# Optimization experiments

Measured on AMD Instinct MI355X. Metric: run time of the kernel, lower is better.

Reference implementation:

```python
import jax, jax.numpy as jnp
import numpy as np

B, S, D = 4, 4096, 1024
EXPAND = 2
D_INNER = EXPAND * D          # 2048
D_CONV = 4
CHUNK = 64
H = 16
DH = D // H                   # 64
EPS = 1e-5


def setup_inputs() -> dict:
    key = jax.random.key(0)
    ks = jax.random.split(key, 10)
    s = 0.02
    return {
        "x": jax.random.normal(ks[0], (B, S, D), jnp.float32),
        "norm_w": jnp.ones((D,), jnp.float32),
        "w_up": jax.random.normal(ks[1], (D, D_INNER), jnp.float32) * s,
        "w_gate": jax.random.normal(ks[2], (D, D_INNER), jnp.float32) * s,
        "w_down": jax.random.normal(ks[3], (D_INNER, D), jnp.float32) * s,
        "conv_w": jax.random.normal(ks[4], (D_INNER, 1, D_CONV), jnp.float32) * s,
        "conv_b": jnp.zeros((D_INNER,), jnp.float32),
        "wq": jax.random.normal(ks[5], (D, D), jnp.float32) * s,
        "wk": jax.random.normal(ks[6], (D, D), jnp.float32) * s,
        "wv": jax.random.normal(ks[7], (D, D), jnp.float32) * s,
        "wo": jax.random.normal(ks[8], (D, D), jnp.float32) * s,
    }


def rmsnorm(x, w):
    var = jnp.mean(jnp.square(x.astype(jnp.float32)), axis=-1, keepdims=True)
    return (x * jax.lax.rsqrt(var + EPS).astype(x.dtype)) * w


def causal_dwconv(x, w, b):
    # x: [B, S, C] -> depthwise causal conv along S
    y = jax.lax.conv_general_dilated(
        x.transpose(0, 2, 1), w,
        window_strides=(1,), padding=[(D_CONV - 1, 0)],
        feature_group_count=D_INNER,
        dimension_numbers=("NCH", "OIH", "NCH"))
    return (y + b[None, :, None]).transpose(0, 2, 1)


def hebbian_memory(h, wq, wk, wv, wo):
    # chunked Hebbian associative memory: M += phi(k)^T v, read y = phi(q) M (+ intra-chunk causal)
    phi = lambda t: jax.nn.elu(t) + 1.0
    q = phi((h @ wq).reshape(B, S, H, DH)) * (DH ** -0.5)
    k = phi((h @ wk).reshape(B, S, H, DH))
    v = (h @ wv).reshape(B, S, H, DH)

    def to_chunks(t):  # [B,S,H,DH] -> [N, B, H, CHUNK, DH]
        return t.reshape(B, S // CHUNK, CHUNK, H, DH).transpose(1, 0, 3, 2, 4)

    qc, kc, vc = to_chunks(q), to_chunks(k), to_chunks(v)
    mask = jnp.tril(jnp.ones((CHUNK, CHUNK), bool))

    def step(M, inp):
        qb, kb, vb = inp                                   # [B,H,C,DH]
        inter = jnp.einsum("bhcd,bhde->bhce", qb, M)       # read from past memory
        sc = jnp.einsum("bhcd,bhed->bhce", qb, kb)
        sc = jnp.where(mask, sc, 0.0)                      # causal intra-chunk Hebbian read
        intra = jnp.einsum("bhce,bhed->bhcd", sc, vb)
        M = M + jnp.einsum("bhcd,bhce->bhde", kb, vb)      # Hebbian outer-product write
        return M, inter + intra

    M0 = jnp.zeros((B, H, DH, DH), h.dtype)
    _, y = jax.lax.scan(step, M0, (qc, kc, vc))            # y: [N,B,H,C,DH]
    y = y.transpose(1, 0, 3, 2, 4).reshape(B, S, D)
    return y @ wo


def reference(x, norm_w, w_up, w_gate, w_down, conv_w, conv_b, wq, wk, wv, wo):
    normed = rmsnorm(x, norm_w)
    val = jax.nn.silu(causal_dwconv(normed @ w_up, conv_w, conv_b))   # conv local mixing
    h = (jax.nn.silu(normed @ w_gate) * val) @ w_down                 # gated MLP
    out = hebbian_memory(h, wq, wk, wv, wo)                           # associative memory
    return x + out
```

## Files before the change

### kernel.cpp

```cpp
#include <hip/hip_runtime.h>
#include <hip/hip_fp16.h>
#include <cstdint>

#define NRALL 16384
#define DM    1024
#define DI    2048
#define SEQL  4096

typedef _Float16 f16;
typedef _Float16 f16x8 __attribute__((ext_vector_type(8)));
typedef _Float16 f16x4 __attribute__((ext_vector_type(4)));
typedef float    f32x4 __attribute__((ext_vector_type(4)));

__device__ __forceinline__ float phi_f(float t)  { return t > 0.0f ? t + 1.0f : __expf(t); }
__device__ __forceinline__ float silu_f(float t) { return t / (1.0f + __expf(-t)); }

#define GLDS16(g, l)                                                            \
    __builtin_amdgcn_global_load_lds(                                           \
        (const __attribute__((address_space(1))) void*)(g),                     \
        (__attribute__((address_space(3))) void*)(l), 16, 0, 0)

#define FMA4(dst, s, vv)                      \
    dst.x = fmaf((s), (vv).x, dst.x);         \
    dst.y = fmaf((s), (vv).y, dst.y);         \
    dst.z = fmaf((s), (vv).z, dst.z);         \
    dst.w = fmaf((s), (vv).w, dst.w;)

__device__ __forceinline__ void wfmt_one(const float* __restrict__ W, char* __restrict__ fmt,
                                         int n, int kt, int Nw, int Ntot, int noff)
{
    const int ng = noff + n;
#pragma unroll
    for (int kh = 0; kh < 2; ++kh) {
        char* o = fmt + ((size_t)(kt * 2 + kh) * Ntot + ng) * 64;
#pragma unroll
        for (int c2 = 0; c2 < 4; ++c2) {
            f16x8 p;
#pragma unroll
            for (int j = 0; j < 8; ++j)
                p[j] = (f16)W[(size_t)(kt * 64 + kh * 32 + c2 * 8 + j) * Nw + n];
            *(f16x8*)(o + ((c2 ^ ((ng >> 1) & 3)) << 4)) = p;
        }
    }
}

__global__ __launch_bounds__(256) void prep_k(const float* __restrict__ x,
                                              const float* __restrict__ nw,
                                              f16* __restrict__ xn,
                                              const float* __restrict__ w_up,
                                              const float* __restrict__ w_gate,
                                              const float* __restrict__ w_down,
                                              const float* __restrict__ wq,
                                              const float* __restrict__ wk,
                                              const float* __restrict__ wv,
                                              const float* __restrict__ wo,
                                              char* __restrict__ fmtUG,
                                              char* __restrict__ fmtD,
                                              char* __restrict__ fmtQKV,
                                              char* __restrict__ fmtO)
{
    const int t = threadIdx.x;
    if (blockIdx.x < NRALL) {
        const int r = blockIdx.x;
        const float4 v = *(const float4*)(x + (size_t)r * DM + t * 4);
        float s = v.x * v.x + v.y * v.y + v.z * v.z + v.w * v.w;
#pragma unroll
        for (int m = 1; m < 64; m <<= 1) s += __shfl_xor(s, m);
        __shared__ float ws4[4];
        if ((t & 63) == 0) ws4[t >> 6] = s;
        __syncthreads();
        const float tot = ws4[0] + ws4[1] + ws4[2] + ws4[3];
        const float sc = rsqrtf(tot * (1.0f / DM) + 1e-5f);
        const float4 w = *(const float4*)(nw + t * 4);
        f16x4 o;
        o[0] = (f16)(v.x * sc * w.x); o[1] = (f16)(v.y * sc * w.y);
        o[2] = (f16)(v.z * sc * w.z); o[3] = (f16)(v.w * sc * w.w);
        *(f16x4*)(xn + (size_t)r * DM + t * 4) = o;
        return;
    }
    int id = blockIdx.x - NRALL;
    if (id < 128) { wfmt_one(w_up,   fmtUG,  (id % 8) * 256 + t, id / 8, DI, 4096, 0);    return; }
    id -= 128;
    if (id < 128) { wfmt_one(w_gate, fmtUG,  (id % 8) * 256 + t, id / 8, DI, 4096, 2048); return; }
    id -= 128;
    if (id < 128) { wfmt_one(w_down, fmtD,   (id % 4) * 256 + t, id / 4, DM, 1024, 0);    return; }
    id -= 128;
    if (id < 64)  { wfmt_one(wq,     fmtQKV, (id % 4) * 256 + t, id / 4, DM, 3072, 0);    return; }
    id -= 64;
    if (id < 64)  { wfmt_one(wk,     fmtQKV, (id % 4) * 256 + t, id / 4, DM, 3072, 1024); return; }
    id -= 64;
    if (id < 64)  { wfmt_one(wv,     fmtQKV, (id % 4) * 256 + t, id / 4, DM, 3072, 2048); return; }
    id -= 64;
    wfmt_one(wo, fmtO, (id % 4) * 256 + t, id / 4, DM, 1024, 0);
}

#define PH(p, ks, mh, STAGE_STMT)                                                 \
    {                                                                             \
        if ((mh) == 0) {                                                          \
            _Pragma("unroll")                                                     \
            for (int q = 0; q < 2; ++q) {                                         \
                const int row = wm * 64 + q * 16 + lr16;                          \
                af[q] = *(const f16x8*)(ldsb + (p) * 32768 + (ks) * 16384         \
                        + row * 64 + ((kb ^ ((row >> 1) & 3)) << 4));             \
            }                                                                     \
            _Pragma("unroll")                                                     \
            for (int q = 0; q < 4; ++q) {                                         \
                const int n = wn * 64 + q * 16 + lr16;                            \
                bf[q] = *(const f16x8*)(ldsb + 65536 + (p) * 32768 + (ks) * 16384 \
                        + n * 64 + ((kb ^ ((n >> 1) & 3)) << 4));                 \
            }                                                                     \
        } else {                                                                  \
            _Pragma("unroll")                                                     \
            for (int q = 0; q < 2; ++q) {                                         \
                const int row = wm * 64 + (q + 2) * 16 + lr16;                    \
                af[2 + q] = *(const f16x8*)(ldsb + (p) * 32768 + (ks) * 16384     \
                            + row * 64 + ((kb ^ ((row >> 1) & 3)) << 4));         \
            }                                                                     \
        }                                                                         \
        STAGE_STMT;                                                               \
        asm volatile("s_waitcnt vmcnt(3)" ::: "memory");                          \
        __builtin_amdgcn_sched_barrier(0);                                        \
        __builtin_amdgcn_s_barrier();                                             \
        asm volatile("s_waitcnt lgkmcnt(0)" ::: "memory");                        \
        __builtin_amdgcn_sched_barrier(0);                                        \
        __builtin_amdgcn_s_setprio(1);                                            \
        _Pragma("unroll")                                                         \
        for (int q = 0; q < 2; ++q) {                                             \
            acc[(mh) * 2 + q][0] = __builtin_amdgcn_mfma_f32_16x16x32_f16(        \
                af[(mh) * 2 + q], bf[0], acc[(mh) * 2 + q][0], 0, 0, 0);          \
            acc[(mh) * 2 + q][1] = __builtin_amdgcn_mfma_f32_16x16x32_f16(        \
                af[(mh) * 2 + q], bf[1], acc[(mh) * 2 + q][1], 0, 0, 0);          \
            acc[(mh) * 2 + q][2] = __builtin_amdgcn_mfma_f32_16x16x32_f16(        \
                af[(mh) * 2 + q], bf[2], acc[(mh) * 2 + q][2], 0, 0, 0);          \
            acc[(mh) * 2 + q][3] = __builtin_amdgcn_mfma_f32_16x16x32_f16(        \
                af[(mh) * 2 + q], bf[3], acc[(mh) * 2 + q][3], 0, 0, 0);          \
        }                                                                         \
        __builtin_amdgcn_s_setprio(0);                                            \
        __builtin_amdgcn_sched_barrier(0);                                        \
    }

template <int EPI>
__global__ __launch_bounds__(1024) void mg256_k(const f16* __restrict__ A, int lda,
                                                const char* __restrict__ fmt,
                                                void* __restrict__ Cv,
                                                int N, int K, int gx,
                                                const float* __restrict__ addx)
{
    __shared__ __align__(16) char ldsb[131072];

    const int t = threadIdx.x;
    int wid = blockIdx.x;
    { const int cpx = gridDim.x >> 3; wid = (wid & 7) * cpx + (wid >> 3); }
    const int bx = wid % gx, by = wid / gx;
    const int bm = by * 256, bn = bx * 256;
    const int lane = t & 63, wv = t >> 6;
    const int wm = wv >> 2, wn = wv & 3;
    const int kb = lane >> 4, lr16 = lane & 15;
    const int NT = K >> 6;

    f32x4 acc[4][4];
#pragma unroll
    for (int i = 0; i < 4; ++i)
#pragma unroll
        for (int j = 0; j < 4; ++j) acc[i][j] = (f32x4)0.0f;

    const int arow = t >> 2;
    const int ac2 = (t & 3) ^ ((arow >> 1) & 3);
    const f16* Abase = A + (size_t)(bm + arow) * lda + ac2 * 8;
    const char* Bbase = fmt + (size_t)bn * 64 + (size_t)t * 16;
    const size_t BKstep = (size_t)N * 64;
    char* ldsT = ldsb + t * 16;

    auto STAGE_A = [&](int p, int kh, int kt) {
        GLDS16(Abase + kt * 64 + kh * 32, ldsT + p * 32768 + kh * 16384);
    };
    auto STAGE_B = [&](int p, int kh, int kt) {
        GLDS16(Bbase + (size_t)(kt * 2 + kh) * BKstep, ldsT + 65536 + p * 32768 + kh * 16384);
    };

    f16x8 af[4], bf[4];

    const int T1 = NT > 1 ? 1 : 0;
    STAGE_B(0, 0, 0); STAGE_A(0, 0, 0);
    STAGE_B(0, 1, 0); STAGE_A(0, 1, 0);
    STAGE_B(1, 0, T1); STAGE_A(1, 0, T1);
    asm volatile("s_waitcnt vmcnt(4)" ::: "memory");
    __builtin_amdgcn_s_barrier();
    __builtin_amdgcn_sched_barrier(0);

    const int NI = NT >> 1;
    for (int i = 0; i < NI; ++i) {
        const int tA = 2 * i + 1 < NT ? 2 * i + 1 : NT - 1;
        const int tB = 2 * i + 2 < NT ? 2 * i + 2 : NT - 1;
        const int tC = 2 * i + 3 < NT ? 2 * i + 3 : NT - 1;
        PH(0, 0, 0, STAGE_B(1, 1, tA))
        PH(0, 0, 1, STAGE_A(1, 1, tA))
        PH(0, 1, 0, STAGE_B(0, 0, tB))
        PH(0, 1, 1, STAGE_A(0, 0, tB))
        PH(1, 0, 0, STAGE_B(0, 1, tB))
        PH(1, 0, 1, STAGE_A(0, 1, tB))
        PH(1, 1, 0, STAGE_B(1, 0, tC))
        PH(1, 1, 1, STAGE_A(1, 0, tC))
    }
    asm volatile("s_waitcnt vmcnt(0)" ::: "memory");

#pragma unroll
    for (int fm = 0; fm < 4; ++fm) {
        const int row0 = bm + wm * 64 + fm * 16 + kb * 4;
#pragma unroll
        for (int fn = 0; fn < 4; ++fn) {
            const int col = bn + wn * 64 + fn * 16 + lr16;
#pragma unroll
            for (int r = 0; r < 4; ++r) {
                float o = acc[fm][fn][r];
                if (EPI == 1) {
                    if (col < DM) o = phi_f(o) * 0.125f;
                    else if (col < 2 * DM) o = phi_f(o);
                }
                if (EPI == 2) {
                    ((float*)Cv)[(size_t)(row0 + r) * N + col] =
                        o + addx[(size_t)(row0 + r) * N + col];
                } else {
                    ((f16*)Cv)[(size_t)(row0 + r) * N + col] = (f16)o;
                }
            }
        }
    }
}

__global__ __launch_bounds__(256) void conv_gate_k(f16* __restrict__ upg,
                                                   const float* __restrict__ cw,
                                                   const float* __restrict__ cb)
{
    const int r0 = blockIdx.x * 16;
    const int c = threadIdx.x * 8;
    float bias[8];
    {
        const float4 b0 = *(const float4*)(cb + c);
        const float4 b1 = *(const float4*)(cb + c + 4);
        bias[0] = b0.x; bias[1] = b0.y; bias[2] = b0.z; bias[3] = b0.w;
        bias[4] = b1.x; bias[5] = b1.y; bias[6] = b1.z; bias[7] = b1.w;
    }
    float tap[8][4];
#pragma unroll
    for (int j = 0; j < 8; ++j)
        *(float4*)tap[j] = *(const float4*)(cw + (size_t)(c + j) * 4);

    const bool lead = (r0 & (SEQL - 1)) == 0;
    f16x8 w0, w1, w2;
    if (lead) {
        w0 = (f16x8)(f16)0; w1 = (f16x8)(f16)0; w2 = (f16x8)(f16)0;
    } else {
        w0 = *(const f16x8*)(upg + (size_t)(r0 - 3) * 4096 + c);
        w1 = *(const f16x8*)(upg + (size_t)(r0 - 2) * 4096 + c);
        w2 = *(const f16x8*)(upg + (size_t)(r0 - 1) * 4096 + c);
    }
#pragma unroll 4
    for (int i = 0; i < 16; ++i) {
        const size_t row = (size_t)(r0 + i);
        const f16x8 w3 = *(const f16x8*)(upg + row * 4096 + c);
        const f16x8 g  = *(const f16x8*)(upg + row * 4096 + 2048 + c);
        f16x8 o;
#pragma unroll
        for (int j = 0; j < 8; ++j) {
            float a = bias[j];
            a = fmaf((float)w0[j], tap[j][0], a);
            a = fmaf((float)w1[j], tap[j][1], a);
            a = fmaf((float)w2[j], tap[j][2], a);
            a = fmaf((float)w3[j], tap[j][3], a);
            o[j] = (f16)(silu_f((float)g[j]) * silu_f(a));
        }
        *(f16x8*)(upg + row * 4096 + 2048 + c) = o;
        w0 = w1; w1 = w2; w2 = w3;
    }
}

__global__ __launch_bounds__(256) void gscan_g_k(const f16* __restrict__ qkv,
                                                 f16* __restrict__ G)
{
    __shared__ float Ks[4096];
    __shared__ float Vs[4096];
    const int t = threadIdx.x, ch = blockIdx.x, h = blockIdx.y, b = blockIdx.z;
    const int r = t >> 2, c16 = (t & 3) * 16;
    const f16* kp = qkv + ((size_t)b * SEQL + ch * 64 + r) * 3072 + DM + h * 64 + c16;
#pragma unroll
    for (int i = 0; i < 2; ++i) {
        const f16x8 kv = *(const f16x8*)(kp + 8 * i);
        const f16x8 vv = *(const f16x8*)(kp + DM + 8 * i);
#pragma unroll
        for (int j = 0; j < 8; ++j) {
            Ks[r * 64 + c16 + 8 * i + j] = (float)kv[j];
            Vs[r * 64 + c16 + 8 * i + j] = (float)vv[j];
        }
    }
    __syncthreads();
    const int d4 = (t >> 4) * 4, e4 = (t & 15) * 4;
    float4 ag[4] = {};
#pragma unroll 4
    for (int c = 0; c < 64; ++c) {
        float ka[4];
        *(float4*)ka = *(const float4*)(Ks + c * 64 + d4);
        const float4 va = *(const float4*)(Vs + c * 64 + e4);
        ag[0].x = fmaf(ka[0], va.x, ag[0].x); ag[0].y = fmaf(ka[0], va.y, ag[0].y);
        ag[0].z = fmaf(ka[0], va.z, ag[0].z); ag[0].w = fmaf(ka[0], va.w, ag[0].w);
        ag[1].x = fmaf(ka[1], va.x, ag[1].x); ag[1].y = fmaf(ka[1], va.y, ag[1].y);
        ag[1].z = fmaf(ka[1], va.z, ag[1].z); ag[1].w = fmaf(ka[1], va.w, ag[1].w);
        ag[2].x = fmaf(ka[2], va.x, ag[2].x); ag[2].y = fmaf(ka[2], va.y, ag[2].y);
        ag[2].z = fmaf(ka[2], va.z, ag[2].z); ag[2].w = fmaf(ka[2], va.w, ag[2].w);
        ag[3].x = fmaf(ka[3], va.x, ag[3].x); ag[3].y = fmaf(ka[3], va.y, ag[3].y);
        ag[3].z = fmaf(ka[3], va.z, ag[3].z); ag[3].w = fmaf(ka[3], va.w, ag[3].w);
    }
    f16* go = G + (((size_t)b * 16 + h) * 64 + ch) * 4096 + d4 * 64 + e4;
#pragma unroll
    for (int i = 0; i < 4; ++i) {
        f16x4 o;
        o[0] = (f16)ag[i].x; o[1] = (f16)ag[i].y;
        o[2] = (f16)ag[i].z; o[3] = (f16)ag[i].w;
        *(f16x4*)(go + i * 64) = o;
    }
}

__global__ __launch_bounds__(256) void gprefix_k(f16* __restrict__ G)
{
    const int bh = blockIdx.x >> 4, sl = blockIdx.x & 15;
    const int idx = sl * 256 + threadIdx.x;
    float run = 0.0f;
    f16* p = G + (size_t)bh * 64 * 4096 + idx;
#pragma unroll 4
    for (int ch = 0; ch < 64; ++ch) {
        const float g = (float)*p;
        *p = (f16)run;
        run += g;
        p += 4096;
    }
}

__global__ __launch_bounds__(256) void gscan_y_k(const f16* __restrict__ qkv,
                                                 const f16* __restrict__ G,
                                                 f16* __restrict__ y)
{
    __shared__ float qT[4096];
    __shared__ float Kd[4096];
    __shared__ float Vs[4096];
    __shared__ float Ms[4096];
    const int t = threadIdx.x, ch = blockIdx.x, h = blockIdx.y, b = blockIdx.z;
    const int r = t >> 2, c16 = (t & 3) * 16;
    const f16* qp = qkv + ((size_t)b * SEQL + ch * 64 + r) * 3072 + h * 64 + c16;
#pragma unroll
    for (int i = 0; i < 2; ++i) {
        const f16x8 qv = *(const f16x8*)(qp + 8 * i);
        const f16x8 kv = *(const f16x8*)(qp + DM + 8 * i);
        const f16x8 vv = *(const f16x8*)(qp + 2 * DM + 8 * i);
#pragma unroll
        for (int j = 0; j < 8; ++j) {
            qT[(c16 + 8 * i + j) * 64 + r] = (float)qv[j];
            Kd[(c16 + 8 * i + j) * 64 + r] = (float)kv[j];
            Vs[r * 64 + c16 + 8 * i + j] = (float)vv[j];
        }
    }
    const f16* mg = G + (((size_t)b * 16 + h) * 64 + ch) * 4096;
#pragma unroll
    for (int i = 0; i < 2; ++i) {
        const f16x8 mv = *(const f16x8*)(mg + t * 16 + 8 * i);
#pragma unroll
        for (int j = 0; j < 8; ++j) Ms[t * 16 + 8 * i + j] = (float)mv[j];
    }
    __syncthreads();

    const int c4 = (t >> 4) * 4, e4 = (t & 15) * 4;
    float sa[4][4] = {}, ya[4][4] = {};
#pragma unroll 2
    for (int d = 0; d < 64; ++d) {
        float a[4], bb[4], m[4];
        *(float4*)a = *(const float4*)(qT + d * 64 + c4);
        *(float4*)bb = *(const float4*)(Kd + d * 64 + e4);
        *(float4*)m = *(const float4*)(Ms + d * 64 + e4);
#pragma unroll
        for (int i = 0; i < 4; ++i)
#pragma unroll
            for (int j = 0; j < 4; ++j) {
                sa[i][j] = fmaf(a[i], bb[j], sa[i][j]);
                ya[i][j] = fmaf(a[i], m[j], ya[i][j]);
            }
    }
#pragma unroll
    for (int i = 0; i < 4; ++i)
#pragma unroll
        for (int j = 0; j < 4; ++j)
            if (e4 + j > c4 + i) sa[i][j] = 0.0f;
    __syncthreads();
#pragma unroll
    for (int i = 0; i < 4; ++i)
#pragma unroll
        for (int j = 0; j < 4; ++j)
            qT[(e4 + j) * 64 + c4 + i] = sa[i][j];
    __syncthreads();
#pragma unroll 2
    for (int e = 0; e < 64; ++e) {
        float a[4], vv[4];
        *(float4*)a = *(const float4*)(qT + e * 64 + c4);
        *(float4*)vv = *(const float4*)(Vs + e * 64 + e4);
#pragma unroll
        for (int i = 0; i < 4; ++i)
#pragma unroll
            for (int j = 0; j < 4; ++j)
                ya[i][j] = fmaf(a[i], vv[j], ya[i][j]);
    }
#pragma unroll
    for (int i = 0; i < 4; ++i) {
        f16x4 o;
        o[0] = (f16)ya[i][0]; o[1] = (f16)ya[i][1];
        o[2] = (f16)ya[i][2]; o[3] = (f16)ya[i][3];
        *(f16x4*)(y + ((size_t)b * SEQL + ch * 64 + c4 + i) * DM + h * 64 + e4) = o;
    }
}

extern "C" void kernel_launch(void* const* d_in, const int* in_sizes, int n_in,
                              void* d_out, int out_size, void* d_ws, size_t ws_size,
                              hipStream_t stream)
{
    const float* x      = (const float*)d_in[0];
    const float* norm_w = (const float*)d_in[1];
    const float* w_up   = (const float*)d_in[2];
    const float* w_gate = (const float*)d_in[3];
    const float* w_down = (const float*)d_in[4];
    const float* conv_w = (const float*)d_in[5];
    const float* conv_b = (const float*)d_in[6];
    const float* wq     = (const float*)d_in[7];
    const float* wk     = (const float*)d_in[8];
    const float* wv     = (const float*)d_in[9];
    const float* wo     = (const float*)d_in[10];
    float* out = (float*)d_out;

    const size_t BIG_NEED = 247463936ull;
    const bool big = ws_size >= BIG_NEED;

    if (big) {
        char* p = (char*)d_ws;
        f16* upg = (f16*)p;               p += (size_t)NRALL * 4096 * 2;
        f16* hb  = (f16*)p;               p += (size_t)NRALL * DM * 2;
        char* fmtD   = p;                 p += (size_t)64 * 1024 * 64;
        char* fmtQKV = p;                 p += (size_t)32 * 3072 * 64;
        char* fmtO   = p;                 p += (size_t)32 * 1024 * 64;
        f16* xn = (f16*)p;                p += (size_t)NRALL * DM * 2;
        char* fmtUG  = p;
        f16* G = (f16*)xn;
        f16* qkvb = upg;
        f16* yb   = hb;

        prep_k<<<NRALL + 640, 256, 0, stream>>>(x, norm_w, xn, w_up, w_gate, w_down,
                                                wq, wk, wv, wo, fmtUG, fmtD, fmtQKV, fmtO);

        mg256_k<0><<<16 * 64, 1024, 0, stream>>>(xn, DM, fmtUG, upg, 4096, DM, 16, nullptr);
        conv_gate_k<<<NRALL / 16, 256, 0, stream>>>(upg, conv_w, conv_b);
        mg256_k<0><<<4 * 64, 1024, 0, stream>>>(upg + 2048, 4096, fmtD, hb, 1024, DI, 4, nullptr);
        mg256_k<1><<<12 * 64, 1024, 0, stream>>>(hb, DM, fmtQKV, qkvb, 3072, DM, 12, nullptr);

        gscan_g_k<<<dim3(64, 16, 4), 256, 0, stream>>>(qkvb, G);
        gprefix_k<<<1024, 256, 0, stream>>>(G);
        gscan_y_k<<<dim3(64, 16, 4), 256, 0, stream>>>(qkvb, G, yb);

        mg256_k<2><<<4 * 64, 1024, 0, stream>>>(yb, DM, fmtO, out, 1024, DM, 4, x);
    } else {
        char* p = (char*)d_ws;
        f16* xn = (f16*)p;                p += (size_t)NRALL * DM * 2;
        f16* upg = (f16*)p;               p += (size_t)SEQL * 4096 * 2;
        f16* hb  = (f16*)p;               p += (size_t)SEQL * DM * 2;
        f16* G = (f16*)p;                 p += (size_t)16 * 64 * 4096 * 2;
        char* fmtUG  = p;                 p += (size_t)32 * 4096 * 64;
        char* fmtD   = p;                 p += (size_t)64 * 1024 * 64;
        char* fmtQKV = p;                 p += (size_t)32 * 3072 * 64;
        char* fmtO   = p;
        f16* qkvb = upg;
        f16* yb   = hb;

        prep_k<<<NRALL + 640, 256, 0, stream>>>(x, norm_w, xn, w_up, w_gate, w_down,
                                                wq, wk, wv, wo, fmtUG, fmtD, fmtQKV, fmtO);

        for (int b = 0; b < 4; ++b) {
            const f16* xnb = xn + (size_t)b * SEQL * DM;
            mg256_k<0><<<16 * 16, 1024, 0, stream>>>(xnb, DM, fmtUG, upg, 4096, DM, 16, nullptr);
            conv_gate_k<<<SEQL / 16, 256, 0, stream>>>(upg, conv_w, conv_b);
            mg256_k<0><<<4 * 16, 1024, 0, stream>>>(upg + 2048, 4096, fmtD, hb, 1024, DI, 4, nullptr);
            mg256_k<1><<<12 * 16, 1024, 0, stream>>>(hb, DM, fmtQKV, qkvb, 3072, DM, 12, nullptr);
            gscan_g_k<<<dim3(64, 16, 1), 256, 0, stream>>>(qkvb, G);
            gprefix_k<<<256, 256, 0, stream>>>(G);
            gscan_y_k<<<dim3(64, 16, 1), 256, 0, stream>>>(qkvb, G, yb);
            mg256_k<2><<<4 * 16, 1024, 0, stream>>>(yb, DM, fmtO,
                                                    out + (size_t)b * SEQL * DM, 1024, DM, 4,
                                                    x + (size_t)b * SEQL * DM);
        }
    }
}
```

Before: 621.6 us.

## Move chunk readout to MFMA with transposed memory state and swizzled f16 LDS

The per-chunk readout kernel now runs its three small matmuls (q·k^T, q·M, S·V) on MFMA 16x16x32 f16 instructions instead of scalar FP32 FMAs. It stages f16 tiles in XOR-swizzled LDS, with V transposed and a masked score tile. To match, the state kernel writes the memory transposed (e-major), and the prefix-sum kernel handles two f16 values per thread with half the blocks. This cuts FP32 ALU work and LDS footprint. In exchange the intra-chunk scores are rounded to f16 before the second matmul, which adds precision risk.

```diff
diff --git a/kernel.cpp b/kernel.cpp
--- a/kernel.cpp
+++ b/kernel.cpp
@@ -10,6 +10,7 @@
 typedef _Float16 f16;
 typedef _Float16 f16x8 __attribute__((ext_vector_type(8)));
 typedef _Float16 f16x4 __attribute__((ext_vector_type(4)));
+typedef _Float16 f16x2 __attribute__((ext_vector_type(2)));
 typedef float    f32x4 __attribute__((ext_vector_type(4)));
 
 __device__ __forceinline__ float phi_f(float t)  { return t > 0.0f ? t + 1.0f : __expf(t); }
@@ -19,12 +20,6 @@
     __builtin_amdgcn_global_load_lds(                                           \
         (const __attribute__((address_space(1))) void*)(g),                     \
         (__attribute__((address_space(3))) void*)(l), 16, 0, 0)
-
-#define FMA4(dst, s, vv)                      \
-    dst.x = fmaf((s), (vv).x, dst.x);         \
-    dst.y = fmaf((s), (vv).y, dst.y);         \
-    dst.z = fmaf((s), (vv).z, dst.z);         \
-    dst.w = fmaf((s), (vv).w, dst.w;)
 
 __device__ __forceinline__ void wfmt_one(const float* __restrict__ W, char* __restrict__ fmt,
                                          int n, int kt, int Nw, int Ntot, int noff)
@@ -276,7 +271,7 @@
 }
 
 __global__ __launch_bounds__(256) void gscan_g_k(const f16* __restrict__ qkv,
-                                                 f16* __restrict__ G)
+                                                 f16* __restrict__ GT)
 {
     __shared__ float Ks[4096];
     __shared__ float Vs[4096];
@@ -294,23 +289,23 @@
         }
     }
     __syncthreads();
-    const int d4 = (t >> 4) * 4, e4 = (t & 15) * 4;
+    const int e4 = (t >> 4) * 4, d4 = (t & 15) * 4;
     float4 ag[4] = {};
 #pragma unroll 4
     for (int c = 0; c < 64; ++c) {
-        float ka[4];
-        *(float4*)ka = *(const float4*)(Ks + c * 64 + d4);
-        const float4 va = *(const float4*)(Vs + c * 64 + e4);
-        ag[0].x = fmaf(ka[0], va.x, ag[0].x); ag[0].y = fmaf(ka[0], va.y, ag[0].y);
-        ag[0].z = fmaf(ka[0], va.z, ag[0].z); ag[0].w = fmaf(ka[0], va.w, ag[0].w);
-        ag[1].x = fmaf(ka[1], va.x, ag[1].x); ag[1].y = fmaf(ka[1], va.y, ag[1].y);
-        ag[1].z = fmaf(ka[1], va.z, ag[1].z); ag[1].w = fmaf(ka[1], va.w, ag[1].w);
-        ag[2].x = fmaf(ka[2], va.x, ag[2].x); ag[2].y = fmaf(ka[2], va.y, ag[2].y);
-        ag[2].z = fmaf(ka[2], va.z, ag[2].z); ag[2].w = fmaf(ka[2], va.w, ag[2].w);
-        ag[3].x = fmaf(ka[3], va.x, ag[3].x); ag[3].y = fmaf(ka[3], va.y, ag[3].y);
-        ag[3].z = fmaf(ka[3], va.z, ag[3].z); ag[3].w = fmaf(ka[3], va.w, ag[3].w);
-    }
-    f16* go = G + (((size_t)b * 16 + h) * 64 + ch) * 4096 + d4 * 64 + e4;
+        float va[4];
+        *(float4*)va = *(const float4*)(Vs + c * 64 + e4);
+        const float4 ka = *(const float4*)(Ks + c * 64 + d4);
+        ag[0].x = fmaf(va[0], ka.x, ag[0].x); ag[0].y = fmaf(va[0], ka.y, ag[0].y);
+        ag[0].z = fmaf(va[0], ka.z, ag[0].z); ag[0].w = fmaf(va[0], ka.w, ag[0].w);
+        ag[1].x = fmaf(va[1], ka.x, ag[1].x); ag[1].y = fmaf(va[1], ka.y, ag[1].y);
+        ag[1].z = fmaf(va[1], ka.z, ag[1].z); ag[1].w = fmaf(va[1], ka.w, ag[1].w);
+        ag[2].x = fmaf(va[2], ka.x, ag[2].x); ag[2].y = fmaf(va[2], ka.y, ag[2].y);
+        ag[2].z = fmaf(va[2], ka.z, ag[2].z); ag[2].w = fmaf(va[2], ka.w, ag[2].w);
+        ag[3].x = fmaf(va[3], ka.x, ag[3].x); ag[3].y = fmaf(va[3], ka.y, ag[3].y);
+        ag[3].z = fmaf(va[3], ka.z, ag[3].z); ag[3].w = fmaf(va[3], ka.w, ag[3].w);
+    }
+    f16* go = GT + (((size_t)b * 16 + h) * 64 + ch) * 4096 + e4 * 64 + d4;
 #pragma unroll
     for (int i = 0; i < 4; ++i) {
         f16x4 o;
@@ -322,97 +317,119 @@
 
 __global__ __launch_bounds__(256) void gprefix_k(f16* __restrict__ G)
 {
-    const int bh = blockIdx.x >> 4, sl = blockIdx.x & 15;
-    const int idx = sl * 256 + threadIdx.x;
-    float run = 0.0f;
-    f16* p = G + (size_t)bh * 64 * 4096 + idx;
+    const int bh = blockIdx.x >> 3, sl = blockIdx.x & 7;
+    f16x2* p = (f16x2*)(G + (size_t)bh * 64 * 4096) + sl * 256 + threadIdx.x;
+    float r0 = 0.0f, r1 = 0.0f;
 #pragma unroll 4
     for (int ch = 0; ch < 64; ++ch) {
-        const float g = (float)*p;
-        *p = (f16)run;
-        run += g;
-        p += 4096;
+        const f16x2 g = *p;
+        f16x2 o; o[0] = (f16)r0; o[1] = (f16)r1;
+        *p = o;
+        r0 += (float)g[0]; r1 += (float)g[1];
+        p += 2048;
     }
 }
 
 __global__ __launch_bounds__(256) void gscan_y_k(const f16* __restrict__ qkv,
-                                                 const f16* __restrict__ G,
+                                                 const f16* __restrict__ GT,
                                                  f16* __restrict__ y)
 {
-    __shared__ float qT[4096];
-    __shared__ float Kd[4096];
-    __shared__ float Vs[4096];
-    __shared__ float Ms[4096];
+    __shared__ __align__(16) char lds[40960];
+    f16* Qs = (f16*)lds;
+    f16* Ks = (f16*)(lds + 8192);
+    f16* Ms = (f16*)(lds + 16384);
+    f16* Vt = (f16*)(lds + 24576);
+    f16* Ss = (f16*)(lds + 32768);
+
     const int t = threadIdx.x, ch = blockIdx.x, h = blockIdx.y, b = blockIdx.z;
-    const int r = t >> 2, c16 = (t & 3) * 16;
-    const f16* qp = qkv + ((size_t)b * SEQL + ch * 64 + r) * 3072 + h * 64 + c16;
-#pragma unroll
-    for (int i = 0; i < 2; ++i) {
-        const f16x8 qv = *(const f16x8*)(qp + 8 * i);
-        const f16x8 kv = *(const f16x8*)(qp + DM + 8 * i);
-        const f16x8 vv = *(const f16x8*)(qp + 2 * DM + 8 * i);
-#pragma unroll
-        for (int j = 0; j < 8; ++j) {
-            qT[(c16 + 8 * i + j) * 64 + r] = (float)qv[j];
-            Kd[(c16 + 8 * i + j) * 64 + r] = (float)kv[j];
-            Vs[r * 64 + c16 + 8 * i + j] = (float)vv[j];
-        }
-    }
-    const f16* mg = G + (((size_t)b * 16 + h) * 64 + ch) * 4096;
-#pragma unroll
-    for (int i = 0; i < 2; ++i) {
-        const f16x8 mv = *(const f16x8*)(mg + t * 16 + 8 * i);
-#pragma unroll
-        for (int j = 0; j < 8; ++j) Ms[t * 16 + 8 * i + j] = (float)mv[j];
+    const int lane = t & 63, w = t >> 6;
+    const int kb = lane >> 4, lr16 = lane & 15;
+
+    const int r = t >> 2;
+    const int c0 = (t & 3) * 2;
+    const int rkey = (r >> 1) & 3;
+    const f16* qp = qkv + ((size_t)b * SEQL + ch * 64 + r) * 3072 + h * 64;
+    const f16* mp = GT + (((size_t)b * 16 + h) * 64 + ch) * 4096 + r * 64;
+#pragma unroll
+    for (int cc = 0; cc < 2; ++cc) {
+        const int c = c0 + cc;
+        const int sw = c ^ rkey;
+        const f16x8 qv = *(const f16x8*)(qp + c * 8);
+        const f16x8 kv = *(const f16x8*)(qp + DM + c * 8);
+        const f16x8 vv = *(const f16x8*)(qp + 2 * DM + c * 8);
+        const f16x8 mv = *(const f16x8*)(mp + c * 8);
+        *(f16x8*)(Qs + r * 64 + sw * 8) = qv;
+        *(f16x8*)(Ks + r * 64 + sw * 8) = kv;
+        *(f16x8*)(Ms + r * 64 + sw * 8) = mv;
+#pragma unroll
+        for (int jj = 0; jj < 8; ++jj) {
+            const int j = c * 8 + jj;
+            Vt[j * 64 + ((((r >> 3) ^ ((j >> 1) & 3)) << 3) + (r & 7))] = vv[jj];
+        }
     }
     __syncthreads();
 
-    const int c4 = (t >> 4) * 4, e4 = (t & 15) * 4;
-    float sa[4][4] = {}, ya[4][4] = {};
-#pragma unroll 2
-    for (int d = 0; d < 64; ++d) {
-        float a[4], bb[4], m[4];
-        *(float4*)a = *(const float4*)(qT + d * 64 + c4);
-        *(float4*)bb = *(const float4*)(Kd + d * 64 + e4);
-        *(float4*)m = *(const float4*)(Ms + d * 64 + e4);
-#pragma unroll
-        for (int i = 0; i < 4; ++i)
-#pragma unroll
-            for (int j = 0; j < 4; ++j) {
-                sa[i][j] = fmaf(a[i], bb[j], sa[i][j]);
-                ya[i][j] = fmaf(a[i], m[j], ya[i][j]);
-            }
-    }
-#pragma unroll
-    for (int i = 0; i < 4; ++i)
-#pragma unroll
-        for (int j = 0; j < 4; ++j)
-            if (e4 + j > c4 + i) sa[i][j] = 0.0f;
+    f16x8 af[2];
+    {
+        const int row = w * 16 + lr16;
+        const int sz = (row >> 1) & 3;
+        af[0] = *(const f16x8*)(Qs + row * 64 + (kb ^ sz) * 8);
+        af[1] = *(const f16x8*)(Qs + row * 64 + (4 + (kb ^ sz)) * 8);
+    }
+    f32x4 accs[4];
+#pragma unroll
+    for (int te = 0; te < 4; ++te) accs[te] = (f32x4)0.0f;
+#pragma unroll
+    for (int te = 0; te < 4; ++te) {
+        const int er = te * 16 + lr16;
+        const int es = (er >> 1) & 3;
+        const f16x8 b0 = *(const f16x8*)(Ks + er * 64 + (kb ^ es) * 8);
+        const f16x8 b1 = *(const f16x8*)(Ks + er * 64 + (4 + (kb ^ es)) * 8);
+        accs[te] = __builtin_amdgcn_mfma_f32_16x16x32_f16(af[0], b0, accs[te], 0, 0, 0);
+        accs[te] = __builtin_amdgcn_mfma_f32_16x16x32_f16(af[1], b1, accs[te], 0, 0, 0);
+    }
+#pragma unroll
+    for (int te = 0; te < 4; ++te)
+#pragma unroll
+        for (int rr = 0; rr < 4; ++rr) {
+            const int rc = w * 16 + kb * 4 + rr;
+            const int ce = te * 16 + lr16;
+            const float v = (ce <= rc) ? accs[te][rr] : 0.0f;
+            Ss[rc * 64 + ((((ce >> 3) ^ ((rc >> 1) & 3)) << 3) + (ce & 7))] = (f16)v;
+        }
     __syncthreads();
-#pragma unroll
-    for (int i = 0; i < 4; ++i)
-#pragma unroll
-        for (int j = 0; j < 4; ++j)
-            qT[(e4 + j) * 64 + c4 + i] = sa[i][j];
-    __syncthreads();
-#pragma unroll 2
-    for (int e = 0; e < 64; ++e) {
-        float a[4], vv[4];
-        *(float4*)a = *(const float4*)(qT + e * 64 + c4);
-        *(float4*)vv = *(const float4*)(Vs + e * 64 + e4);
-#pragma unroll
-        for (int i = 0; i < 4; ++i)
-#pragma unroll
-            for (int j = 0; j < 4; ++j)
-                ya[i][j] = fmaf(a[i], vv[j], ya[i][j]);
-    }
-#pragma unroll
-    for (int i = 0; i < 4; ++i) {
-        f16x4 o;
-        o[0] = (f16)ya[i][0]; o[1] = (f16)ya[i][1];
-        o[2] = (f16)ya[i][2]; o[3] = (f16)ya[i][3];
-        *(f16x4*)(y + ((size_t)b * SEQL + ch * 64 + c4 + i) * DM + h * 64 + e4) = o;
-    }
+
+    f16x8 as2[2];
+    {
+        const int row = w * 16 + lr16;
+        const int sz = (row >> 1) & 3;
+        as2[0] = *(const f16x8*)(Ss + row * 64 + (kb ^ sz) * 8);
+        as2[1] = *(const f16x8*)(Ss + row * 64 + (4 + (kb ^ sz)) * 8);
+    }
+    f32x4 accy[4];
+#pragma unroll
+    for (int tj = 0; tj < 4; ++tj) accy[tj] = (f32x4)0.0f;
+#pragma unroll
+    for (int tj = 0; tj < 4; ++tj) {
+        const int jr = tj * 16 + lr16;
+        const int js = (jr >> 1) & 3;
+        const f16x8 m0 = *(const f16x8*)(Ms + jr * 64 + (kb ^ js) * 8);
+        const f16x8 m1 = *(const f16x8*)(Ms + jr * 64 + (4 + (kb ^ js)) * 8);
+        const f16x8 v0 = *(const f16x8*)(Vt + jr * 64 + (kb ^ js) * 8);
+        const f16x8 v1 = *(const f16x8*)(Vt + jr * 64 + (4 + (kb ^ js)) * 8);
+        accy[tj] = __builtin_amdgcn_mfma_f32_16x16x32_f16(af[0],  m0, accy[tj], 0, 0, 0);
+        accy[tj] = __builtin_amdgcn_mfma_f32_16x16x32_f16(af[1],  m1, accy[tj], 0, 0, 0);
+        accy[tj] = __builtin_amdgcn_mfma_f32_16x16x32_f16(as2[0], v0, accy[tj], 0, 0, 0);
+        accy[tj] = __builtin_amdgcn_mfma_f32_16x16x32_f16(as2[1], v1, accy[tj], 0, 0, 0);
+    }
+    f16* yo = y + ((size_t)b * SEQL + ch * 64) * DM + h * 64;
+#pragma unroll
+    for (int tj = 0; tj < 4; ++tj)
+#pragma unroll
+        for (int rr = 0; rr < 4; ++rr) {
+            const int rc = w * 16 + kb * 4 + rr;
+            yo[(size_t)rc * DM + tj * 16 + lr16] = (f16)accy[tj][rr];
+        }
 }
 
 extern "C" void kernel_launch(void* const* d_in, const int* in_sizes, int n_in,
@@ -457,7 +474,7 @@
         mg256_k<1><<<12 * 64, 1024, 0, stream>>>(hb, DM, fmtQKV, qkvb, 3072, DM, 12, nullptr);
 
         gscan_g_k<<<dim3(64, 16, 4), 256, 0, stream>>>(qkvb, G);
-        gprefix_k<<<1024, 256, 0, stream>>>(G);
+        gprefix_k<<<512, 256, 0, stream>>>(G);
         gscan_y_k<<<dim3(64, 16, 4), 256, 0, stream>>>(qkvb, G, yb);
 
         mg256_k<2><<<4 * 64, 1024, 0, stream>>>(yb, DM, fmtO, out, 1024, DM, 4, x);
@@ -484,7 +501,7 @@
             mg256_k<0><<<4 * 16, 1024, 0, stream>>>(upg + 2048, 4096, fmtD, hb, 1024, DI, 4, nullptr);
             mg256_k<1><<<12 * 16, 1024, 0, stream>>>(hb, DM, fmtQKV, qkvb, 3072, DM, 12, nullptr);
             gscan_g_k<<<dim3(64, 16, 1), 256, 0, stream>>>(qkvb, G);
-            gprefix_k<<<256, 256, 0, stream>>>(G);
+            gprefix_k<<<128, 256, 0, stream>>>(G);
             gscan_y_k<<<dim3(64, 16, 1), 256, 0, stream>>>(qkvb, G, yb);
             mg256_k<2><<<4 * 16, 1024, 0, stream>>>(yb, DM, fmtO,
                                                     out + (size_t)b * SEQL * DM, 1024, DM, 4,
```

New measurement: 533.2 us, median of 2. -14.2%, faster.
